# Optimization experiments

Hardware: AMD Instinct MI355X
Metric: run time of the kernel (lower is better)

## Reference

```python
import jax, jax.numpy as jnp
import numpy as np

EPS = 1e-5  # PNA std-aggregator epsilon
N_NODES, N_EDGES, F_DIM, N_LAYERS = 50000, 800000, 64, 3


def setup_inputs() -> dict:
    key = jax.random.key(0)
    ks = jax.random.split(key, 6)
    x = jax.random.normal(ks[0], (N_NODES, F_DIM), jnp.float32)
    edge_index = jax.random.randint(ks[1], (2, N_EDGES), 0, N_NODES, jnp.int32)
    # Per-layer parameters, stacked on a leading layer axis.
    pre_w = jax.random.normal(ks[2], (N_LAYERS, 2 * F_DIM, F_DIM), jnp.float32) / np.sqrt(2 * F_DIM).astype(np.float32)
    pre_b = jnp.zeros((N_LAYERS, F_DIM), jnp.float32)
    post_w = jax.random.normal(ks[3], (N_LAYERS, 13 * F_DIM, F_DIM), jnp.float32) / np.sqrt(13 * F_DIM).astype(np.float32)
    post_b = jnp.zeros((N_LAYERS, F_DIM), jnp.float32)
    lin_w = jax.random.normal(ks[4], (N_LAYERS, F_DIM, F_DIM), jnp.float32) / np.sqrt(F_DIM).astype(np.float32)
    lin_b = jnpp = jnp.zeros((N_LAYERS, F_DIM), jnp.float32)
    return dict(x=x, edge_index=edge_index, pre_w=pre_w, pre_b=pre_b,
                post_w=post_w, post_b=post_b, lin_w=lin_w, lin_b=lin_b)


def reference(x, edge_index, pre_w, pre_b, post_w, post_b, lin_w, lin_b):
    src, dst = edge_index[0], edge_index[1]
    n = x.shape[0]
    # In-degree of aggregation targets (clamped to >=1, as in PyG DegreeScalerAggregation).
    deg = jax.ops.segment_sum(jnp.ones_like(dst, dtype=x.dtype), dst, num_segments=n)
    has_edge = (deg > 0)[:, None]
    deg_c = jnp.maximum(deg, 1.0)[:, None]              # [N,1]
    log_deg = jnp.log(deg_c + 1.0)                      # [N,1]
    avg_log = jnp.mean(log_deg)
    amp = log_deg / avg_log                              # amplification scaler
    att = avg_log / log_deg                              # attenuation scaler

    h = x
    for l in range(pre_w.shape[0]):
        # message: pre_nn(cat([x_i, x_j]))  -> [E, F]
        m = jnp.concatenate([h[dst], h[src]], axis=-1) @ pre_w[l] + pre_b[l]
        # fused multi-aggregator scatter-reduce per target node
        s1 = jax.ops.segment_sum(m, dst, num_segments=n)
        s2 = jax.ops.segment_sum(m * m, dst, num_segments=n)
        mean = s1 / deg_c
        std = jnp.sqrt(jax.nn.relu(s2 / deg_c - mean * mean) + EPS)
        mx = jnp.where(has_edge, jax.ops.segment_max(m, dst, num_segments=n), 0.0)
        mn = jnp.where(has_edge, jax.ops.segment_min(m, dst, num_segments=n), 0.0)
        agg = jnp.concatenate([mean, mx, mn, std], axis=-1)        # [N, 4F]
        scaled = jnp.concatenate([agg, agg * amp, agg * att], -1)  # [N, 12F]
        # post_nn(cat([x, scaled])) then final lin, plus residual shortcut
        out = jnp.concatenate([h, scaled], axis=-1) @ post_w[l] + post_b[l]
        out = out @ lin_w[l] + lin_b[l]
        h = out + h
    return h
```

## Files before the change

kernel.cpp:

```cpp
#include <hip/hip_runtime.h>
#include <math.h>

#define EPSV 1e-5f
#define EPB3 4096
#define NBP 256
#define CAP 6144

typedef short s16x8 __attribute__((ext_vector_type(8)));
typedef float f32x4 __attribute__((ext_vector_type(4)));
typedef unsigned short u16;
typedef unsigned short u16x4 __attribute__((ext_vector_type(4)));

#define MFMA(a, b, c) __builtin_amdgcn_mfma_f32_16x16x32_bf16(a, b, c, 0, 0, 0)

__device__ inline u16 f2bf(float f) {
    unsigned u = __float_as_uint(f);
    return (u16)((u + 0x7FFF + ((u >> 16) & 1)) >> 16);
}
__device__ inline float bf2f(u16 h) { return __uint_as_float(((unsigned)h) << 16); }

__device__ inline void split8(const float4& a, const float4& b, s16x8& hv, s16x8& lv) {
    float f[8] = {a.x, a.y, a.z, a.w, b.x, b.y, b.z, b.w};
#pragma unroll
    for (int i = 0; i < 8; ++i) {
        u16 h = f2bf(f[i]);
        hv[i] = (short)h;
        lv[i] = (short)f2bf(f[i] - bf2f(h));
    }
}


__global__ void k_wprep(const float* __restrict__ pre_w, const float* __restrict__ post_w,
                        const float* __restrict__ post_b, const float* __restrict__ lin_w,
                        const float* __restrict__ lin_b, u16* __restrict__ WpT_hi,
                        u16* __restrict__ WpT_lo, u16* __restrict__ WT_hi,
                        u16* __restrict__ WT_lo, float* __restrict__ bpp,
                        int* __restrict__ bucketCur, float* __restrict__ lsum) {
    int l = blockIdx.y, bx = blockIdx.x, t = threadIdx.x;
    if (bx < 320) {
        int k = bx, j = t;
        int third = j >> 6, c = j & 63;
        float out = 0.f;
        int r = -1;
        if (k < 64) r = (third == 0) ? k : -1;
        else        r = 64 + third * 256 + (k - 64);
        if (r >= 0) {
            const float* pw = post_w + (size_t)(l * 832 + r) * 64;
            const float* lw = lin_w + (size_t)l * 64 * 64;
            float s = 0.f;
            for (int kk = 0; kk < 64; ++kk) s += pw[kk] * lw[kk * 64 + c];
            out = s;
        }
        u16 h = f2bf(out);
        size_t o = ((size_t)l * 192 + j) * 320 + k;
        WT_hi[o] = h;
        WT_lo[o] = f2bf(out - bf2f(h));
    } else if (bx < 448) {
        if (t < 64) {
            int c = bx - 320, k = t;
            float v = pre_w[(size_t)l * 8192 + (size_t)(k + (c >= 64 ? 64 : 0)) * 64 + (c & 63)];
            u16 h = f2bf(v);
            size_t o = ((size_t)l * 128 + c) * 64 + k;
            WpT_hi[o] = h;
            WpT_lo[o] = f2bf(v - bf2f(h));
        }
    } else if (bx == 448) {
        if (t < 64) {
            int c = t;
            const float* pb = post_b + l * 64;
            const float* lw = lin_w + (size_t)l * 64 * 64;
            float s = lin_b[l * 64 + c];
            for (int k = 0; k < 64; ++k) s += pb[k] * lw[k * 64 + c];
            bpp[l * 64 + c] = s;
        }
    } else if (l == 0) {
        int i = (bx - 449) * 192 + t;
        if (i < NBP) bucketCur[i] = 0;
        if (i == 0) *lsum = 0.f;
    }
}

__global__ __launch_bounds__(512) void k_bucket3(const int* __restrict__ src,
                                                 const int* __restrict__ dst, int E,
                                                 int* __restrict__ bucketCursor,
                                                 unsigned* __restrict__ edgeTmp) {
    __shared__ int cnt[NBP], loff[NBP], lpos[NBP], gbase[NBP], sbuf[NBP];
    __shared__ unsigned stage[EPB3];
    int t = threadIdx.x;
    int base = blockIdx.x * EPB3;
    int cntE = min(EPB3, E - base);
    if (t < NBP) cnt[t] = 0;
    __syncthreads();
    unsigned ed[8];
#pragma unroll
    for (int j = 0; j < 8; ++j) {
        int idx = j * 512 + t;
        if (idx < cntE) {
            int e = base + idx;
            unsigned s = (unsigned)src[e];
            unsigned d = (unsigned)dst[e];
            ed[j] = ((d >> 8) << 24) | ((d & 255u) << 16) | s;
            atomicAdd(&cnt[d >> 8], 1);
        } else ed[j] = 0xFFFFFFFFu;
    }
    __syncthreads();
    if (t < NBP) sbuf[t] = cnt[t];
    __syncthreads();
    for (int o = 1; o < NBP; o <<= 1) {
        int v = 0;
        if (t < NBP && t >= o) v = sbuf[t - o];
        __syncthreads();
        if (t < NBP) sbuf[t] += v;
        __syncthreads();
    }
    if (t < NBP) {
        loff[t] = sbuf[t] - cnt[t];
        lpos[t] = sbuf[t] - cnt[t];
        gbase[t] = (cnt[t] > 0) ? atomicAdd(&bucketCursor[t], cnt[t]) : 0;
    }
    __syncthreads();
#pragma unroll
    for (int j = 0; j < 8; ++j) {
        if (ed[j] != 0xFFFFFFFFu) {
            int b = ed[j] >> 24;
            int p = atomicAdd(&lpos[b], 1);
            stage[p] = ed[j];
        }
    }
    __syncthreads();
    for (int i = t; i < cntE; i += 512) {
        unsigned pr = stage[i];
        int b = pr >> 24;
        int pos = gbase[b] + (i - loff[b]);
        if (pos < CAP) edgeTmp[(size_t)b * CAP + pos] = pr;
    }
}

__global__ __launch_bounds__(512) void k_csort2(const unsigned* __restrict__ edgeTmp,
                                                const int* __restrict__ bucketCur,
                                                int* __restrict__ deg,
                                                int* __restrict__ offs,
                                                float* __restrict__ lsum,
                                                u16* __restrict__ srcSorted,
                                                int N, int E, int NB) {
    __shared__ int bcnt[NBP], sbuf[NBP], lcur[NBP], lofs[NBP];
    __shared__ float fred[256];
    __shared__ u16 stageSrc[CAP];
    __shared__ int e0s;
    int b = blockIdx.x, t = threadIdx.x;
    int n0 = b << 8;
    int nodes = min(256, N - n0);
    if (t < NBP) bcnt[t] = (t < NB) ? bucketCur[t] : 0;
    if (t < NBP) lcur[t] = 0;
    __syncthreads();
    if (t < NBP) sbuf[t] = bcnt[t];
    __syncthreads();
    for (int o = 1; o < NBP; o <<= 1) {
        int v = 0;
        if (t < NBP && t >= o) v = sbuf[t - o];
        __syncthreads();
        if (t < NBP) sbuf[t] += v;
        __syncthreads();
    }
    if (t == 0) e0s = sbuf[b] - bcnt[b];
    __syncthreads();
    int e0 = e0s;
    int cnt = min(bcnt[b], CAP);
    const unsigned* ebase = edgeTmp + (size_t)b * CAP;
    for (int i = t; i < cnt; i += 512) atomicAdd(&lcur[(ebase[i] >> 16) & 255], 1);
    __syncthreads();
    float ls = 0.f;
    if (t < 256) {
        if (t < nodes) {
            int d = lcur[t];
            deg[n0 + t] = d;
            ls = logf(fmaxf((float)d, 1.f) + 1.f);
        }
        fred[t] = ls;
    }
    if (t < NBP) sbuf[t] = lcur[t];
    __syncthreads();
    for (int o = 1; o < NBP; o <<= 1) {
        int v = 0;
        if (t < NBP && t >= o) v = sbuf[t - o];
        __syncthreads();
        if (t < NBP) sbuf[t] += v;
        __syncthreads();
    }
    if (t < NBP) lofs[t] = sbuf[t] - lcur[t];
    if (t < nodes) offs[n0 + t] = e0 + (sbuf[t] - lcur[t]);
    if (b == 0 && t == 0) offs[N] = E;
    __syncthreads();
    for (int o = 128; o > 0; o >>= 1) {
        if (t < o) fred[t] += fred[t + o];
        __syncthreads();
    }
    if (t == 0) atomicAdd(lsum, fred[0]);
    if (t < NBP) sbuf[t] = 0;
    __syncthreads();
    for (int i = t; i < cnt; i += 512) {
        unsigned p = ebase[i];
        int dl = (p >> 16) & 255;
        int r = atomicAdd(&sbuf[dl], 1);
        stageSrc[lofs[dl] + r] = (u16)(p & 0xFFFFu);
    }
    __syncthreads();
    for (int i = t; i < cnt; i += 512) srcSorted[e0 + i] = stageSrc[i];
}


__global__ __launch_bounds__(256) void k_gemm1(const float* __restrict__ h,
                                               const u16* __restrict__ WpT_hi,
                                               const u16* __restrict__ WpT_lo,
                                               const float* __restrict__ pre_b,
                                               u16* __restrict__ Ph, u16* __restrict__ Qh,
                                               int M) {
    __shared__ u16 Ah[64 * 72], Al[64 * 72];
    __shared__ u16 Bh[128 * 72], Bl[128 * 72];
    int t = threadIdx.x, wid = t >> 6, lane = t & 63;
    int rows0 = blockIdx.x * 64;
    int quad = lane >> 4, l16 = lane & 15;
    int wm = wid & 1, wn = wid >> 1;

#pragma unroll
    for (int it = 0; it < 2; ++it) {
        int task = it * 256 + t;
        int r = task >> 3, seg = task & 7;
        int row = rows0 + r;
        float4 v0 = make_float4(0.f, 0.f, 0.f, 0.f), v1 = v0;
        if (row < M) {
            v0 = *(const float4*)&h[(size_t)row * 64 + seg * 8];
            v1 = *(const float4*)&h[(size_t)row * 64 + seg * 8 + 4];
        }
        s16x8 hv, lv;
        split8(v0, v1, hv, lv);
        *(s16x8*)&Ah[r * 72 + seg * 8] = hv;
        *(s16x8*)&Al[r * 72 + seg * 8] = lv;
    }
#pragma unroll
    for (int it = 0; it < 4; ++it) {
        int task = it * 256 + t;
        int c = task >> 3, seg = task & 7;
        *(s16x8*)&Bh[c * 72 + seg * 8] = *(const s16x8*)&WpT_hi[(size_t)c * 64 + seg * 8];
        *(s16x8*)&Bl[c * 72 + seg * 8] = *(const s16x8*)&WpT_lo[(size_t)c * 64 + seg * 8];
    }
    __syncthreads();

    f32x4 acc[2][4];
#pragma unroll
    for (int mt = 0; mt < 2; ++mt)
#pragma unroll
        for (int tt = 0; tt < 4; ++tt) acc[mt][tt] = (f32x4){0.f, 0.f, 0.f, 0.f};

#pragma unroll
    for (int c = 0; c < 2; ++c) {
        s16x8 ah[2], al[2];
#pragma unroll
        for (int mt = 0; mt < 2; ++mt) {
            int r = wm * 32 + mt * 16 + l16;
            ah[mt] = *(s16x8*)&Ah[r * 72 + c * 32 + quad * 8];
            al[mt] = *(s16x8*)&Al[r * 72 + c * 32 + quad * 8];
        }
#pragma unroll
        for (int tt = 0; tt < 4; ++tt) {
            int cc = wn * 64 + tt * 16 + l16;
            s16x8 bh = *(s16x8*)&Bh[cc * 72 + c * 32 + quad * 8];
            s16x8 bl = *(s16x8*)&Bl[cc * 72 + c * 32 + quad * 8];
#pragma unroll
            for (int mt = 0; mt < 2; ++mt) {
                acc[mt][tt] = MFMA(ah[mt], bh, acc[mt][tt]);
                acc[mt][tt] = MFMA(ah[mt], bl, acc[mt][tt]);
                if (wn == 0) acc[mt][tt] = MFMA(al[mt], bh, acc[mt][tt]);
            }
        }
    }

#pragma unroll
    for (int mt = 0; mt < 2; ++mt)
#pragma unroll
        for (int tt = 0; tt < 4; ++tt) {
            int col = wn * 64 + tt * 16 + l16;
#pragma unroll
            for (int r = 0; r < 4; ++r) {
                int row = rows0 + wm * 32 + mt * 16 + quad * 4 + r;
                if (row >= M) continue;
                float v = acc[mt][tt][r];
                if (col < 64) Ph[(size_t)row * 64 + col] = f2bf(v + pre_b[col]);
                else          Qh[(size_t)row * 64 + (col - 64)] = f2bf(v);
            }
        }
}

__global__ __launch_bounds__(256) void k_agg(const u16* __restrict__ Ph,
                                             const u16* __restrict__ Qh,
                                             const int* __restrict__ offs,
                                             const u16* __restrict__ ss,
                                             u16* __restrict__ AGGh, int N) {
    int w = threadIdx.x >> 6, lane = threadIdx.x & 63;
    int g = lane >> 4;
    int f4b = (lane & 15) << 3;
    int node = blockIdx.x * 16 + w * 4 + g;
    int nc = min(node, N - 1);
    int beg = offs[nc], end = offs[nc + 1];
    int deg = (node < N) ? (end - beg) : 0;
    end = beg + deg;
    int mdeg = deg;
    mdeg = max(mdeg, __shfl_xor(mdeg, 16));
    mdeg = max(mdeg, __shfl_xor(mdeg, 32));

    float sum0 = 0.f, sum1 = 0.f, sum2 = 0.f, sum3 = 0.f;
    float sq0 = 0.f, sq1 = 0.f, sq2 = 0.f, sq3 = 0.f;
    float mx0 = -3.4e38f, mx1 = -3.4e38f, mx2 = -3.4e38f, mx3 = -3.4e38f;
    float mn0 = 3.4e38f, mn1 = 3.4e38f, mn2 = 3.4e38f, mn3 = 3.4e38f;

    const char* qbase = (const char*)Qh;

#define ACC4(LO, HI)                                                        \
    {                                                                       \
        float q0 = __uint_as_float((LO) << 16);                             \
        float q1 = __uint_as_float((LO) & 0xFFFF0000u);                     \
        float q2 = __uint_as_float((HI) << 16);                             \
        float q3 = __uint_as_float((HI) & 0xFFFF0000u);                     \
        sum0 += q0; sq0 = fmaf(q0, q0, sq0);                                \
        mx0 = fmaxf(mx0, q0); mn0 = fminf(mn0, q0);                         \
        sum1 += q1; sq1 = fmaf(q1, q1, sq1);                                \
        mx1 = fmaxf(mx1, q1); mn1 = fminf(mn1, q1);                         \
        sum2 += q2; sq2 = fmaf(q2, q2, sq2);                                \
        mx2 = fmaxf(mx2, q2); mn2 = fminf(mn2, q2);                         \
        sum3 += q3; sq3 = fmaf(q3, q3, sq3);                                \
        mx3 = fmaxf(mx3, q3); mn3 = fminf(mn3, q3);                         \
    }

    int e = beg;
    for (int it = 0; it < mdeg; it += 2) {
        if (e + 1 < end) {
            unsigned s0 = ss[e];
            unsigned s1 = ss[e + 1];
            uint2 a = *(const uint2*)(qbase + ((s0 << 7) | f4b));
            uint2 b = *(const uint2*)(qbase + ((s1 << 7) | f4b));
            ACC4(a.x, a.y);
            ACC4(b.x, b.y);
            e += 2;
        } else if (e < end) {
            unsigned s0 = ss[e];
            uint2 a = *(const uint2*)(qbase + ((s0 << 7) | f4b));
            ACC4(a.x, a.y);
            e += 1;
        }
    }
#undef ACC4

    float dc = fmaxf((float)deg, 1.f);
    float inv = 1.0f / dc;
    float e0 = sum0 * inv, e1 = sum1 * inv, e2 = sum2 * inv, e3 = sum3 * inv;
    float sd0 = sqrtf(fmaxf(fmaf(-e0, e0, sq0 * inv), 0.f) + EPSV);
    float sd1 = sqrtf(fmaxf(fmaf(-e1, e1, sq1 * inv), 0.f) + EPSV);
    float sd2 = sqrtf(fmaxf(fmaf(-e2, e2, sq2 * inv), 0.f) + EPSV);
    float sd3 = sqrtf(fmaxf(fmaf(-e3, e3, sq3 * inv), 0.f) + EPSV);

    uint2 pw = *(const uint2*)((const char*)Ph + ((nc << 7) | f4b));
    float p0 = __uint_as_float(pw.x << 16), p1 = __uint_as_float(pw.x & 0xFFFF0000u);
    float p2 = __uint_as_float(pw.y << 16), p3 = __uint_as_float(pw.y & 0xFFFF0000u);

    bool he = deg > 0;
    float m0 = he ? p0 + e0 : 0.f, m1 = he ? p1 + e1 : 0.f;
    float m2 = he ? p2 + e2 : 0.f, m3 = he ? p3 + e3 : 0.f;
    float X0 = he ? p0 + mx0 : 0.f, X1 = he ? p1 + mx1 : 0.f;
    float X2 = he ? p2 + mx2 : 0.f, X3 = he ? p3 + mx3 : 0.f;
    float n0 = he ? p0 + mn0 : 0.f, n1 = he ? p1 + mn1 : 0.f;
    float n2 = he ? p2 + mn2 : 0.f, n3 = he ? p3 + mn3 : 0.f;

    if (node < N) {
        u16* out = (u16*)((char*)AGGh + (((unsigned)node << 9) | f4b));
        *(u16x4*)(out)       = (u16x4){f2bf(m0), f2bf(m1), f2bf(m2), f2bf(m3)};
        *(u16x4*)(out + 64)  = (u16x4){f2bf(X0), f2bf(X1), f2bf(X2), f2bf(X3)};
        *(u16x4*)(out + 128) = (u16x4){f2bf(n0), f2bf(n1), f2bf(n2), f2bf(n3)};
        *(u16x4*)(out + 192) = (u16x4){f2bf(sd0), f2bf(sd1), f2bf(sd2), f2bf(sd3)};
    }
}

__global__ __launch_bounds__(512) void k_gemm2(const float* __restrict__ hIn,
                                               const u16* __restrict__ AGGh,
                                               const u16* __restrict__ WT_hi,
                                               const u16* __restrict__ WT_lo,
                                               const float* __restrict__ bpp,
                                               const int* __restrict__ degp,
                                               const float* __restrict__ lsum,
                                               float* __restrict__ hOut,
                                               int doNext,
                                               const u16* __restrict__ WpN_hi,
                                               const u16* __restrict__ WpN_lo,
                                               const float* __restrict__ pre_bN,
                                               u16* __restrict__ PhN,
                                               u16* __restrict__ QhN, int M) {
    __shared__ u16 Ah[128 * 40], Al[128 * 40];
    __shared__ u16 Bh[192 * 40], Bl[192 * 40];
    int t = threadIdx.x, wid = t >> 6, lane = t & 63;
    int rows0 = blockIdx.x * 128;
    int quad = lane >> 4, l16 = lane & 15;
    int wm = wid & 3, wn = wid >> 2;

    f32x4 acc[2][6];
#pragma unroll
    for (int mt = 0; mt < 2; ++mt)
#pragma unroll
        for (int tt = 0; tt < 6; ++tt) acc[mt][tt] = (f32x4){0.f, 0.f, 0.f, 0.f};

#pragma unroll
    for (int chunk = 0; chunk < 2; ++chunk) {
        {
            int r = t >> 2, seg = t & 3;
            int row = rows0 + r;
            float4 v0 = make_float4(0.f, 0.f, 0.f, 0.f), v1 = v0;
            if (row < M) {
                v0 = *(const float4*)&hIn[(size_t)row * 64 + chunk * 32 + seg * 8];
                v1 = *(const float4*)&hIn[(size_t)row * 64 + chunk * 32 + seg * 8 + 4];
            }
            s16x8 hv, lv;
            split8(v0, v1, hv, lv);
            *(s16x8*)&Ah[r * 40 + seg * 8] = hv;
            *(s16x8*)&Al[r * 40 + seg * 8] = lv;
        }
        if (t < 256) {
            int c = t >> 2, seg = t & 3;
            int k0g = chunk * 32;
            *(s16x8*)&Bh[c * 40 + seg * 8] = *(const s16x8*)&WT_hi[(size_t)c * 320 + k0g + seg * 8];
            *(s16x8*)&Bl[c * 40 + seg * 8] = *(const s16x8*)&WT_lo[(size_t)c * 320 + k0g + seg * 8];
        }
        __syncthreads();

        s16x8 ah[2], al[2];
#pragma unroll
        for (int mt = 0; mt < 2; ++mt) {
            int r = wm * 32 + mt * 16 + l16;
            ah[mt] = *(s16x8*)&Ah[r * 40 + quad * 8];
            al[mt] = *(s16x8*)&Al[r * 40 + quad * 8];
        }
#pragma unroll
        for (int cg = 0; cg < 2; ++cg) {
            int cc = wn * 32 + cg * 16 + l16;
            s16x8 bh = *(s16x8*)&Bh[cc * 40 + quad * 8];
            s16x8 bl = *(s16x8*)&Bl[cc * 40 + quad * 8];
#pragma unroll
            for (int mt = 0; mt < 2; ++mt) {
                acc[mt][cg] = MFMA(ah[mt], bh, acc[mt][cg]);
                acc[mt][cg] = MFMA(al[mt], bh, acc[mt][cg]);
                acc[mt][cg] = MFMA(ah[mt], bl, acc[mt][cg]);
            }
        }
        __syncthreads();
    }

    for (int chunk = 0; chunk < 8; ++chunk) {
        {
            int r = t >> 2, seg = t & 3;
            int row = rows0 + r;
            s16x8 v = (s16x8){0, 0, 0, 0, 0, 0, 0, 0};
            if (row < M) v = *(const s16x8*)&AGGh[(size_t)row * 256 + chunk * 32 + seg * 8];
            *(s16x8*)&Ah[r * 40 + seg * 8] = v;
        }
        {
            int k0g = 64 + chunk * 32;
#pragma unroll
            for (int it = 0; it < 2; ++it) {
                int task = it * 512 + t;
                if (task < 768) {
                    int c = task >> 2, seg = task & 3;
                    *(s16x8*)&Bh[c * 40 + seg * 8] = *(const s16x8*)&WT_hi[(size_t)c * 320 + k0g + seg * 8];
                    *(s16x8*)&Bl[c * 40 + seg * 8] = *(const s16x8*)&WT_lo[(size_t)c * 320 + k0g + seg * 8];
                }
            }
        }
        __syncthreads();

        s16x8 ah[2];
#pragma unroll
        for (int mt = 0; mt < 2; ++mt) {
            int r = wm * 32 + mt * 16 + l16;
            ah[mt] = *(s16x8*)&Ah[r * 40 + quad * 8];
        }
#pragma unroll
        for (int tt = 0; tt < 6; ++tt) {
            int cc = wn * 32 + (tt & 1) * 16 + (tt >> 1) * 64 + l16;
            s16x8 bh = *(s16x8*)&Bh[cc * 40 + quad * 8];
            s16x8 bl = *(s16x8*)&Bl[cc * 40 + quad * 8];
#pragma unroll
            for (int mt = 0; mt < 2; ++mt) {
                acc[mt][tt] = MFMA(ah[mt], bh, acc[mt][tt]);
                acc[mt][tt] = MFMA(ah[mt], bl, acc[mt][tt]);
            }
        }
        __syncthreads();
    }

    float hv[2][2][4];
    float avg = *lsum / (float)M;
#pragma unroll
    for (int mt = 0; mt < 2; ++mt)
#pragma unroll
        for (int r = 0; r < 4; ++r) {
            int row = rows0 + wm * 32 + mt * 16 + quad * 4 + r;
            float am = 1.f, at = 1.f, hin0 = 0.f, hin1 = 0.f;
            if (row < M) {
                float dc = fmaxf((float)degp[row], 1.f);
                float ld = logf(dc + 1.f);
                am = ld / avg;
                at = avg / ld;
                hin0 = hIn[(size_t)row * 64 + wn * 32 + l16];
                hin1 = hIn[(size_t)row * 64 + wn * 32 + 16 + l16];
            }
#pragma unroll
            for (int cg = 0; cg < 2; ++cg) {
                int col = wn * 32 + cg * 16 + l16;
                float v = acc[mt][cg][r] + am * acc[mt][cg + 2][r] + at * acc[mt][cg + 4][r]
                        + (cg == 0 ? hin0 : hin1) + bpp[col];
                hv[mt][cg][r] = v;
                if (row < M) hOut[(size_t)row * 64 + col] = v;
            }
        }

    if (doNext) {
        f32x4 acc2[2][4];
#pragma unroll
        for (int mt = 0; mt < 2; ++mt)
#pragma unroll
            for (int tt = 0; tt < 4; ++tt) acc2[mt][tt] = (f32x4){0.f, 0.f, 0.f, 0.f};

#pragma unroll
        for (int chunk = 0; chunk < 2; ++chunk) {
            {
                int c = t >> 2, seg = t & 3;
                *(s16x8*)&Bh[c * 40 + seg * 8] = *(const s16x8*)&WpN_hi[(size_t)c * 64 + chunk * 32 + seg * 8];
                *(s16x8*)&Bl[c * 40 + seg * 8] = *(const s16x8*)&WpN_lo[(size_t)c * 64 + chunk * 32 + seg * 8];
            }
            if (wn == chunk) {
#pragma unroll
                for (int mt = 0; mt < 2; ++mt)
#pragma unroll
                    for (int cg = 0; cg < 2; ++cg) {
                        int lc = cg * 16 + l16;
#pragma unroll
                        for (int r = 0; r < 4; ++r) {
                            int rl = wm * 32 + mt * 16 + quad * 4 + r;
                            float v = hv[mt][cg][r];
                            u16 hi = f2bf(v);
                            Ah[rl * 40 + lc] = hi;
                            Al[rl * 40 + lc] = f2bf(v - bf2f(hi));
                        }
                    }
            }
            __syncthreads();

            s16x8 ah[2], al[2];
#pragma unroll
            for (int mt = 0; mt < 2; ++mt) {
                int r = wm * 32 + mt * 16 + l16;
                ah[mt] = *(s16x8*)&Ah[r * 40 + quad * 8];
                al[mt] = *(s16x8*)&Al[r * 40 + quad * 8];
            }
#pragma unroll
            for (int tt = 0; tt < 4; ++tt) {
                int cc = wn * 64 + tt * 16 + l16;
                s16x8 bh = *(s16x8*)&Bh[cc * 40 + quad * 8];
                s16x8 bl = *(s16x8*)&Bl[cc * 40 + quad * 8];
#pragma unroll
                for (int mt = 0; mt < 2; ++mt) {
                    acc2[mt][tt] = MFMA(ah[mt], bh, acc2[mt][tt]);
                    acc2[mt][tt] = MFMA(ah[mt], bl, acc2[mt][tt]);
                    if (wn == 0) acc2[mt][tt] = MFMA(al[mt], bh, acc2[mt][tt]);
                }
            }
            __syncthreads();
        }

#pragma unroll
        for (int mt = 0; mt < 2; ++mt)
#pragma unroll
            for (int tt = 0; tt < 4; ++tt) {
                int col = wn * 64 + tt * 16 + l16;
#pragma unroll
                for (int r = 0; r < 4; ++r) {
                    int row = rows0 + wm * 32 + mt * 16 + quad * 4 + r;
                    if (row >= M) continue;
                    float v = acc2[mt][tt][r];
                    if (col < 64) PhN[(size_t)row * 64 + col] = f2bf(v + pre_bN[col]);
                    else          QhN[(size_t)row * 64 + (col - 64)] = f2bf(v);
                }
            }
    }
}


extern "C" void kernel_launch(void* const* d_in, const int* in_sizes, int n_in,
                              void* d_out, int out_size, void* d_ws, size_t ws_size,
                              hipStream_t stream) {
    const float* x      = (const float*)d_in[0];
    const int*   ei     = (const int*)d_in[1];
    const float* pre_w  = (const float*)d_in[2];
    const float* pre_b  = (const float*)d_in[3];
    const float* post_w = (const float*)d_in[4];
    const float* post_b = (const float*)d_in[5];
    const float* lin_w  = (const float*)d_in[6];
    const float* lin_b  = (const float*)d_in[7];

    const int N = in_sizes[0] / 64;
    const int E = in_sizes[1] / 2;
    const int L = in_sizes[2] / (128 * 64);

    const int* srcIdx = ei;
    const int* dstIdx = ei + E;

    char* ws = (char*)d_ws;
    size_t off = 0;
    auto alloc = [&](size_t bytes) {
        void* p = ws + off;
        off += (bytes + 255) & ~(size_t)255;
        return p;
    };
    int*      deg        = (int*)alloc((size_t)N * 4);
    int*      offs       = (int*)alloc((size_t)(N + 1) * 4);
    u16*      srcSorted  = (u16*)alloc((size_t)E * 2);
    unsigned* edgeTmp    = (unsigned*)alloc((size_t)NBP * CAP * 4);
    int*      bucketCur  = (int*)alloc(NBP * 4);
    float*    lsum       = (float*)alloc(256);
    u16*      WpT_hi     = (u16*)alloc((size_t)L * 128 * 64 * 2);
    u16*      WpT_lo     = (u16*)alloc((size_t)L * 128 * 64 * 2);
    u16*      WT_hi      = (u16*)alloc((size_t)L * 192 * 320 * 2);
    u16*      WT_lo      = (u16*)alloc((size_t)L * 192 * 320 * 2);
    float*    bpp        = (float*)alloc((size_t)L * 64 * 4);
    u16*      Ph         = (u16*)alloc((size_t)N * 64 * 2);
    u16*      Qh         = (u16*)alloc((size_t)N * 64 * 2);
    u16*      AGGh       = (u16*)alloc((size_t)N * 256 * 2);
    float*    hA         = (float*)alloc((size_t)N * 64 * 4);
    float*    hB         = (float*)alloc((size_t)N * 64 * 4);
    (void)ws_size;

    int NB = (N + 255) >> 8;
    int NB1 = (E + EPB3 - 1) / EPB3;
    int initBlk = (NBP + 191) / 192;

    k_wprep<<<dim3(449 + initBlk, L), 192, 0, stream>>>(
        pre_w, post_w, post_b, lin_w, lin_b, WpT_hi, WpT_lo, WT_hi, WT_lo, bpp,
        bucketCur, lsum);
    k_bucket3<<<NB1, 512, 0, stream>>>(srcIdx, dstIdx, E, bucketCur, edgeTmp);
    k_csort2<<<NB, 512, 0, stream>>>(edgeTmp, bucketCur, deg, offs, lsum,
                                     srcSorted, N, E, NB);

    int gblk = (N + 63) / 64;
    int gblk2 = (N + 127) / 128;
    k_gemm1<<<gblk, 256, 0, stream>>>(x, WpT_hi, WpT_lo, pre_b, Ph, Qh, N);

    const float* hIn = x;
    float* hbuf[2] = {hA, hB};
    for (int l = 0; l < L; ++l) {
        float* hOut = (l == L - 1) ? (float*)d_out : hbuf[l & 1];
        int dn = (l < L - 1) ? 1 : 0;
        int ln = dn ? (l + 1) : 0;
        k_agg<<<(N + 15) / 16, 256, 0, stream>>>(Ph, Qh, offs, srcSorted, AGGh, N);
        k_gemm2<<<gblk2, 512, 0, stream>>>(hIn, AGGh,
                                           WT_hi + (size_t)l * 192 * 320,
                                           WT_lo + (size_t)l * 192 * 320,
                                           bpp + (size_t)l * 64,
                                           deg, lsum, hOut, dn,
                                           WpT_hi + (size_t)ln * 128 * 64,
                                           WpT_lo + (size_t)ln * 128 * 64,
                                           pre_b + (size_t)ln * 64,
                                           Ph, Qh, N);
        hIn = hOut;
    }
}
```

Before: 296.5 us.

## Pad per-node CSR edge lists to multiples of four for vectorized aggregation

The counting sort now lays out each node's source list padded to a multiple of four, filling the padding with the last real neighbor, at a fixed per-bucket stride. This drops the global prefix over buckets. The aggregation kernel reads four source indices per 8-byte load and gathers four neighbor rows per iteration with no per-edge branch. It then subtracts the duplicated padding contributions from sum and sum-of-squares; max and min are unaffected by duplicates. The cost is extra gathers for padding entries and a larger index buffer, and buckets near capacity could overflow the padded stride.

New measurement: 277.0 us. 1.07x faster.

```diff
diff --git a/kernel.cpp b/kernel.cpp
--- a/kernel.cpp
+++ b/kernel.cpp
@@ -5,6 +5,7 @@
 #define EPB3 4096
 #define NBP 256
 #define CAP 6144
+#define CAPS (CAP + 768)
 
 typedef short s16x8 __attribute__((ext_vector_type(8)));
 typedef float f32x4 __attribute__((ext_vector_type(4)));
@@ -143,17 +144,29 @@
                                                 float* __restrict__ lsum,
                                                 u16* __restrict__ srcSorted,
                                                 int N, int E, int NB) {
-    __shared__ int bcnt[NBP], sbuf[NBP], lcur[NBP], lofs[NBP];
+    __shared__ int scnt[NBP], sbuf[NBP], lcur[NBP], lofs[NBP];
     __shared__ float fred[256];
-    __shared__ u16 stageSrc[CAP];
-    __shared__ int e0s;
+    __shared__ u16 stageSrc[CAPS];
+    __shared__ int cntPs;
     int b = blockIdx.x, t = threadIdx.x;
     int n0 = b << 8;
     int nodes = min(256, N - n0);
-    if (t < NBP) bcnt[t] = (t < NB) ? bucketCur[t] : 0;
-    if (t < NBP) lcur[t] = 0;
-    __syncthreads();
-    if (t < NBP) sbuf[t] = bcnt[t];
+    if (t < NBP) { lcur[t] = 0; scnt[t] = 0; }
+    __syncthreads();
+    int cnt = min(bucketCur[b], CAP);
+    const unsigned* ebase = edgeTmp + (size_t)b * CAP;
+    for (int i = t; i < cnt; i += 512) atomicAdd(&lcur[(ebase[i] >> 16) & 255], 1);
+    __syncthreads();
+    float ls = 0.f;
+    int d = 0, dP = 0;
+    if (t < nodes) {
+        d = lcur[t];
+        deg[n0 + t] = d;
+        ls = logf(fmaxf((float)d, 1.f) + 1.f);
+        dP = (d + 3) & ~3;
+    }
+    if (t < 256) fred[t] = ls;
+    if (t < NBP) sbuf[t] = dP;
     __syncthreads();
     for (int o = 1; o < NBP; o <<= 1) {
         int v = 0;
@@ -162,50 +175,30 @@
         if (t < NBP) sbuf[t] += v;
         __syncthreads();
     }
-    if (t == 0) e0s = sbuf[b] - bcnt[b];
-    __syncthreads();
-    int e0 = e0s;
-    int cnt = min(bcnt[b], CAP);
-    const unsigned* ebase = edgeTmp + (size_t)b * CAP;
-    for (int i = t; i < cnt; i += 512) atomicAdd(&lcur[(ebase[i] >> 16) & 255], 1);
-    __syncthreads();
-    float ls = 0.f;
-    if (t < 256) {
-        if (t < nodes) {
-            int d = lcur[t];
-            deg[n0 + t] = d;
-            ls = logf(fmaxf((float)d, 1.f) + 1.f);
-        }
-        fred[t] = ls;
-    }
-    if (t < NBP) sbuf[t] = lcur[t];
-    __syncthreads();
-    for (int o = 1; o < NBP; o <<= 1) {
-        int v = 0;
-        if (t < NBP && t >= o) v = sbuf[t - o];
-        __syncthreads();
-        if (t < NBP) sbuf[t] += v;
-        __syncthreads();
-    }
-    if (t < NBP) lofs[t] = sbuf[t] - lcur[t];
-    if (t < nodes) offs[n0 + t] = e0 + (sbuf[t] - lcur[t]);
-    if (b == 0 && t == 0) offs[N] = E;
+    if (t < NBP) lofs[t] = sbuf[t] - dP;
+    if (t < nodes) offs[n0 + t] = b * CAPS + (sbuf[t] - dP);
+    if (t == NBP - 1) cntPs = sbuf[t];
     __syncthreads();
     for (int o = 128; o > 0; o >>= 1) {
         if (t < o) fred[t] += fred[t + o];
         __syncthreads();
     }
     if (t == 0) atomicAdd(lsum, fred[0]);
-    if (t < NBP) sbuf[t] = 0;
-    __syncthreads();
     for (int i = t; i < cnt; i += 512) {
         unsigned p = ebase[i];
         int dl = (p >> 16) & 255;
-        int r = atomicAdd(&sbuf[dl], 1);
+        int r = atomicAdd(&scnt[dl], 1);
         stageSrc[lofs[dl] + r] = (u16)(p & 0xFFFFu);
     }
     __syncthreads();
-    for (int i = t; i < cnt; i += 512) srcSorted[e0 + i] = stageSrc[i];
+    if (t < nodes && (d & 3)) {
+        int lp = lofs[t];
+        u16 lastv = stageSrc[lp + d - 1];
+        for (int k = d; k < dP; ++k) stageSrc[lp + k] = lastv;
+    }
+    __syncthreads();
+    int cntP = cntPs;
+    for (int i = t; i < cntP; i += 512) srcSorted[(size_t)b * CAPS + i] = stageSrc[i];
 }
 
 
@@ -294,6 +287,7 @@
 __global__ __launch_bounds__(256) void k_agg(const u16* __restrict__ Ph,
                                              const u16* __restrict__ Qh,
                                              const int* __restrict__ offs,
+                                             const int* __restrict__ degp,
                                              const u16* __restrict__ ss,
                                              u16* __restrict__ AGGh, int N) {
     int w = threadIdx.x >> 6, lane = threadIdx.x & 63;
@@ -301,12 +295,14 @@
     int f4b = (lane & 15) << 3;
     int node = blockIdx.x * 16 + w * 4 + g;
     int nc = min(node, N - 1);
-    int beg = offs[nc], end = offs[nc + 1];
-    int deg = (node < N) ? (end - beg) : 0;
-    end = beg + deg;
-    int mdeg = deg;
-    mdeg = max(mdeg, __shfl_xor(mdeg, 16));
-    mdeg = max(mdeg, __shfl_xor(mdeg, 32));
+    int beg = offs[nc];
+    int d = (node < N) ? degp[nc] : 0;
+    int dP = (d + 3) & ~3;
+    int end = beg + dP;
+    int mdP = dP;
+    mdP = max(mdP, __shfl_xor(mdP, 16));
+    mdP = max(mdP, __shfl_xor(mdP, 32));
+    int trips = mdP >> 2;
 
     float sum0 = 0.f, sum1 = 0.f, sum2 = 0.f, sum3 = 0.f;
     float sq0 = 0.f, sq1 = 0.f, sq2 = 0.f, sq3 = 0.f;
@@ -332,25 +328,41 @@
     }
 
     int e = beg;
-    for (int it = 0; it < mdeg; it += 2) {
-        if (e + 1 < end) {
-            unsigned s0 = ss[e];
-            unsigned s1 = ss[e + 1];
-            uint2 a = *(const uint2*)(qbase + ((s0 << 7) | f4b));
-            uint2 b = *(const uint2*)(qbase + ((s1 << 7) | f4b));
-            ACC4(a.x, a.y);
-            ACC4(b.x, b.y);
-            e += 2;
-        } else if (e < end) {
-            unsigned s0 = ss[e];
-            uint2 a = *(const uint2*)(qbase + ((s0 << 7) | f4b));
-            ACC4(a.x, a.y);
-            e += 1;
+    for (int it = 0; it < trips; ++it, e += 4) {
+        if (e < end) {
+            uint2 sw = *(const uint2*)(ss + e);
+            unsigned a0 = ((sw.x & 0xFFFFu) << 7) | (unsigned)f4b;
+            unsigned a1 = ((sw.x >> 16) << 7) | (unsigned)f4b;
+            unsigned a2 = ((sw.y & 0xFFFFu) << 7) | (unsigned)f4b;
+            unsigned a3 = ((sw.y >> 16) << 7) | (unsigned)f4b;
+            uint2 qa = *(const uint2*)(qbase + a0);
+            uint2 qb = *(const uint2*)(qbase + a1);
+            uint2 qc = *(const uint2*)(qbase + a2);
+            uint2 qd = *(const uint2*)(qbase + a3);
+            ACC4(qa.x, qa.y);
+            ACC4(qb.x, qb.y);
+            ACC4(qc.x, qc.y);
+            ACC4(qd.x, qd.y);
         }
     }
 #undef ACC4
 
-    float dc = fmaxf((float)deg, 1.f);
+    if (d & 3) {
+        unsigned sl = ss[beg + d - 1];
+        uint2 ql = *(const uint2*)(qbase + ((sl << 7) | (unsigned)f4b));
+        float padf = (float)(dP - d);
+        float qL0 = __uint_as_float(ql.x << 16);
+        float qL1 = __uint_as_float(ql.x & 0xFFFF0000u);
+        float qL2 = __uint_as_float(ql.y << 16);
+        float qL3 = __uint_as_float(ql.y & 0xFFFF0000u);
+        float t0 = padf * qL0, t1 = padf * qL1, t2 = padf * qL2, t3 = padf * qL3;
+        sum0 -= t0; sq0 = fmaf(-t0, qL0, sq0);
+        sum1 -= t1; sq1 = fmaf(-t1, qL1, sq1);
+        sum2 -= t2; sq2 = fmaf(-t2, qL2, sq2);
+        sum3 -= t3; sq3 = fmaf(-t3, qL3, sq3);
+    }
+
+    float dc = fmaxf((float)d, 1.f);
     float inv = 1.0f / dc;
     float e0 = sum0 * inv, e1 = sum1 * inv, e2 = sum2 * inv, e3 = sum3 * inv;
     float sd0 = sqrtf(fmaxf(fmaf(-e0, e0, sq0 * inv), 0.f) + EPSV);
@@ -358,11 +370,11 @@
     float sd2 = sqrtf(fmaxf(fmaf(-e2, e2, sq2 * inv), 0.f) + EPSV);
     float sd3 = sqrtf(fmaxf(fmaf(-e3, e3, sq3 * inv), 0.f) + EPSV);
 
-    uint2 pw = *(const uint2*)((const char*)Ph + ((nc << 7) | f4b));
+    uint2 pw = *(const uint2*)((const char*)Ph + (((unsigned)nc << 7) | (unsigned)f4b));
     float p0 = __uint_as_float(pw.x << 16), p1 = __uint_as_float(pw.x & 0xFFFF0000u);
     float p2 = __uint_as_float(pw.y << 16), p3 = __uint_as_float(pw.y & 0xFFFF0000u);
 
-    bool he = deg > 0;
+    bool he = d > 0;
     float m0 = he ? p0 + e0 : 0.f, m1 = he ? p1 + e1 : 0.f;
     float m2 = he ? p2 + e2 : 0.f, m3 = he ? p3 + e3 : 0.f;
     float X0 = he ? p0 + mx0 : 0.f, X1 = he ? p1 + mx1 : 0.f;
@@ -371,7 +383,7 @@
     float n2 = he ? p2 + mn2 : 0.f, n3 = he ? p3 + mn3 : 0.f;
 
     if (node < N) {
-        u16* out = (u16*)((char*)AGGh + (((unsigned)node << 9) | f4b));
+        u16* out = (u16*)((char*)AGGh + (((unsigned)node << 9) | (unsigned)f4b));
         *(u16x4*)(out)       = (u16x4){f2bf(m0), f2bf(m1), f2bf(m2), f2bf(m3)};
         *(u16x4*)(out + 64)  = (u16x4){f2bf(X0), f2bf(X1), f2bf(X2), f2bf(X3)};
         *(u16x4*)(out + 128) = (u16x4){f2bf(n0), f2bf(n1), f2bf(n2), f2bf(n3)};
@@ -619,7 +631,7 @@
     };
     int*      deg        = (int*)alloc((size_t)N * 4);
     int*      offs       = (int*)alloc((size_t)(N + 1) * 4);
-    u16*      srcSorted  = (u16*)alloc((size_t)E * 2);
+    u16*      srcSorted  = (u16*)alloc((size_t)NBP * CAPS * 2);
     unsigned* edgeTmp    = (unsigned*)alloc((size_t)NBP * CAP * 4);
     int*      bucketCur  = (int*)alloc(NBP * 4);
     float*    lsum       = (float*)alloc(256);
@@ -656,7 +668,7 @@
         float* hOut = (l == L - 1) ? (float*)d_out : hbuf[l & 1];
         int dn = (l < L - 1) ? 1 : 0;
         int ln = dn ? (l + 1) : 0;
-        k_agg<<<(N + 15) / 16, 256, 0, stream>>>(Ph, Qh, offs, srcSorted, AGGh, N);
+        k_agg<<<(N + 15) / 16, 256, 0, stream>>>(Ph, Qh, offs, deg, srcSorted, AGGh, N);
         k_gemm2<<<gblk2, 512, 0, stream>>>(hIn, AGGh,
                                            WT_hi + (size_t)l * 192 * 320,
                                            WT_lo + (size_t)l * 192 * 320,
```
